# Performance work log

Measured on AMD Instinct MI355X. Metric: run time of the kernel, lower is better.

## Reference

```python
import jax, jax.numpy as jnp
import numpy as np

B, N, H, NH, P = 32, 400, 512, 8, 3
DK = H // NH
SCALE = DK ** -0.5
EPS = 1e-5


def _ln(x, g, b):
    m = jnp.mean(x, axis=-1, keepdims=True)
    v = jnp.mean((x - m) ** 2, axis=-1, keepdims=True)
    return (x - m) * jax.lax.rsqrt(v + EPS) * g + b


def _split(x):  # [B,N,H] -> [B,h,N,dk]
    return x.reshape(x.shape[0], x.shape[1], NH, DK).transpose(0, 2, 1, 3)


def _merge(x):  # [B,h,N,dk] -> [B,N,H]
    return x.transpose(0, 2, 1, 3).reshape(x.shape[0], x.shape[2], H)


def _attn(q, k, v, mask):
    s = jnp.einsum('bhid,bhjd->bhij', q, k) * SCALE
    s = s * (1.0 + mask[:, None])  # learned multiplicative prior mask
    p = jax.nn.softmax(s, axis=-1)
    return jnp.einsum('bhij,bhjd->bhid', p, v)


def _weight_gen(pri, z, C, wq, keys, wf, bf):
    # pooled token query attends over the num_priors prior matrices
    qv = jnp.mean(z @ wq, axis=1)  # [B,H]
    aw = jax.nn.softmax((qv @ keys.T) * (H ** -0.5), axis=-1)  # [B,P]
    w = jnp.einsum('bp,bpij->bij', aw, pri)  # [B,N,N] fused prior mask
    fused = jnp.einsum('bij,bjh->bih', C, z) @ wf + bf  # [B,N,H] neighborhood fusion
    return w, aw, fused


def _ffn(x, w1, b1, w2, b2):
    return jax.nn.gelu(x @ w1 + b1, approximate=False) @ w2 + b2


def _forward(x_FC, x_SC, pri_FC, pri_SC, FC, SC, dw,
             ln_attn_FC_g, ln_attn_FC_b, ln_attn_SC_g, ln_attn_SC_b,
             ln_ffn_FC_g, ln_ffn_FC_b, ln_ffn_SC_g, ln_ffn_SC_b,
             qkv_FC_w, qkv_SC_w,
             ffn_FC_w1, ffn_FC_b1, ffn_FC_w2, ffn_FC_b2,
             ffn_SC_w1, ffn_SC_b1, ffn_SC_w2, ffn_SC_b2,
             wg_q_w, wg_keys, wg_fuse_w, wg_fuse_b,
             dist_in_FC_w, dist_in_FC_b, dist_in_SC_w, dist_in_SC_b,
             dist_out_FC_w, dist_out_FC_b, dist_out_SC_w, dist_out_SC_b):
    z_FC = _ln(x_FC, ln_attn_FC_g, ln_attn_FC_b)
    z_SC = _ln(x_SC, ln_attn_SC_g, ln_attn_SC_b)
    q_FC, k_FC, v_FC = [_split(t) for t in jnp.split(z_FC @ qkv_FC_w, 3, axis=-1)]
    q_SC, k_SC, v_SC = [_split(t) for t in jnp.split(z_SC @ qkv_SC_w, 3, axis=-1)]
    w_FC, aw_FC, fused_FC = _weight_gen(pri_FC, z_FC, FC, wg_q_w, wg_keys, wg_fuse_w, wg_fuse_b)
    w_SC, aw_SC, fused_SC = _weight_gen(pri_SC, z_SC, SC, wg_q_w, wg_keys, wg_fuse_w, wg_fuse_b)
    ctx_FC = _merge(_attn(q_FC, k_FC, v_FC, w_FC))
    ctx_SC = _merge(_attn(q_SC, k_SC, v_SC, w_SC))
    attn_out_FC = x_FC + ctx_FC + fused_FC
    attn_out_SC = x_SC + ctx_SC + fused_SC
    x_FC_new = attn_out_FC + _ffn(_ln(attn_out_FC, ln_ffn_FC_g, ln_ffn_FC_b), ffn_FC_w1, ffn_FC_b1, ffn_FC_w2, ffn_FC_b2)
    x_SC_new = attn_out_SC + _ffn(_ln(attn_out_SC, ln_ffn_SC_g, ln_ffn_SC_b), ffn_SC_w1, ffn_SC_b1, ffn_SC_w2, ffn_SC_b2)
    wf, ws = dw[0], dw[1]
    proj_FC = x_FC_new @ dist_in_FC_w + dist_in_FC_b
    proj_SC = x_SC_new @ dist_in_SC_w + dist_in_SC_b
    l_FC = jax.nn.log_softmax(proj_FC.reshape(-1, H), axis=-1)
    l_SC = jax.nn.log_softmax(proj_SC.reshape(-1, H), axis=-1)
    p_FC = jnp.exp(l_FC)
    p_SC = jnp.exp(l_SC)
    rows = jnp.float32(l_FC.shape[0])
    kl_FC = jnp.sum(p_SC * (l_SC - l_FC)) / rows  # KLDiv(batchmean)(l_FC, p_SC)
    kl_SC = jnp.sum(p_FC * (l_FC - l_SC)) / rows
    x_FC_out = (1.0 - wf) * x_FC_new + wf * (proj_FC @ dist_out_FC_w + dist_out_FC_b)
    x_SC_out = (1.0 - ws) * x_SC_new + ws * (proj_SC @ dist_out_SC_w + dist_out_SC_b)
    distill_loss = 0.5 * (kl_FC * wf + kl_SC * ws)
    return (x_FC_out, x_SC_out, distill_loss, aw_FC, aw_SC)


def setup_inputs() -> dict:
    key = jax.random.key(0)
    ks = jax.random.split(key, 24)
    init = lambda k, shape: 0.02 * jax.random.normal(k, shape, jnp.float32)
    d = {}
    d['x_FC'] = jax.random.normal(ks[0], (B, N, H), jnp.float32)
    d['x_SC'] = jax.random.normal(ks[1], (B, N, H), jnp.float32)
    d['pri_FC'] = jax.random.uniform(ks[2], (B, P, N, N), jnp.float32)
    d['pri_SC'] = jax.random.uniform(ks[3], (B, P, N, N), jnp.float32)
    d['FC'] = jax.random.uniform(ks[4], (B, N, N), jnp.float32)
    d['SC'] = jax.random.uniform(ks[5], (B, N, N), jnp.float32)
    d['dw'] = jnp.array([0.5, 0.5], jnp.float32)
    for nm in ['ln_attn_FC', 'ln_attn_SC', 'ln_ffn_FC', 'ln_ffn_SC']:
        d[nm + '_g'] = jnp.ones((H,), jnp.float32)
        d[nm + '_b'] = jnp.zeros((H,), jnp.float32)
    d['qkv_FC_w'] = init(ks[6], (H, 3 * H))
    d['qkv_SC_w'] = init(ks[7], (H, 3 * H))
    d['ffn_FC_w1'] = init(ks[8], (H, 4 * H)); d['ffn_FC_b1'] = jnp.zeros((4 * H,), jnp.float32)
    d['ffn_FC_w2'] = init(ks[9], (4 * H, H)); d['ffn_FC_b2'] = jnp.zeros((H,), jnp.float32)
    d['ffn_SC_w1'] = init(ks[10], (H, 4 * H)); d['ffn_SC_b1'] = jnp.zeros((4 * H,), jnp.float32)
    d['ffn_SC_w2'] = init(ks[11], (4 * H, H)); d['ffn_SC_b2'] = jnp.zeros((H,), jnp.float32)
    d['wg_q_w'] = init(ks[12], (H, H))
    d['wg_keys'] = init(ks[13], (P, H))
    d['wg_fuse_w'] = init(ks[14], (H, H)); d['wg_fuse_b'] = jnp.zeros((H,), jnp.float32)
    d['dist_in_FC_w'] = init(ks[15], (H, H)); d['dist_in_FC_b'] = jnp.zeros((H,), jnp.float32)
    d['dist_in_SC_w'] = init(ks[16], (H, H)); d['dist_in_SC_b'] = jnp.zeros((H,), jnp.float32)
    d['dist_out_FC_w'] = init(ks[17], (H, H)); d['dist_out_FC_b'] = jnp.zeros((H,), jnp.float32)
    d['dist_out_SC_w'] = init(ks[18], (H, H)); d['dist_out_SC_b'] = jnp.zeros((H,), jnp.float32)
    return d


def reference(x_FC, x_SC, pri_FC, pri_SC, FC, SC, dw,
              ln_attn_FC_g, ln_attn_FC_b, ln_attn_SC_g, ln_attn_SC_b,
              ln_ffn_FC_g, ln_ffn_FC_b, ln_ffn_SC_g, ln_ffn_SC_b,
              qkv_FC_w, qkv_SC_w,
              ffn_FC_w1, ffn_FC_b1, ffn_FC_w2, ffn_FC_b2,
              ffn_SC_w1, ffn_SC_b1, ffn_SC_w2, ffn_SC_b2,
              wg_q_w, wg_keys, wg_fuse_w, wg_fuse_b,
              dist_in_FC_w, dist_in_FC_b, dist_in_SC_w, dist_in_SC_b,
              dist_out_FC_w, dist_out_FC_b, dist_out_SC_w, dist_out_SC_b):
    return _forward(x_FC, x_SC, pri_FC, pri_SC, FC, SC, dw,
                    ln_attn_FC_g, ln_attn_FC_b, ln_attn_SC_g, ln_attn_SC_b,
                    ln_ffn_FC_g, ln_ffn_FC_b, ln_ffn_SC_g, ln_ffn_SC_b,
                    qkv_FC_w, qkv_SC_w,
                    ffn_FC_w1, ffn_FC_b1, ffn_FC_w2, ffn_FC_b2,
                    ffn_SC_w1, ffn_SC_b1, ffn_SC_w2, ffn_SC_b2,
                    wg_q_w, wg_keys, wg_fuse_w, wg_fuse_b,
                    dist_in_FC_w, dist_in_FC_b, dist_in_SC_w, dist_in_SC_b,
                    dist_out_FC_w, dist_out_FC_b, dist_out_SC_w, dist_out_SC_b)
```

## Files before the change

### kernel.cpp

```cpp
#include <hip/hip_runtime.h>
#include <hip/hip_bf16.h>
#include <math.h>

typedef __hip_bfloat16 bf16;

#define B_  32
#define N_  400
#define H_  512
#define NH_ 8
#define DK_ 64
#define P_  3
#define BN_ (B_*N_)
#define H3_ 1536
#define H4_ 2048

#define GLD16(g, l) __builtin_amdgcn_global_load_lds( \
    (__attribute__((address_space(1))) void*)(g), \
    (__attribute__((address_space(3))) void*)(l), 16, 0, 0)

__device__ __forceinline__ float b2f(bf16 v){ return __bfloat162float(v); }
__device__ __forceinline__ bf16  f2b(float v){ return __float2bfloat16(v); }
__device__ __forceinline__ float bfu(unsigned short u){ return __uint_as_float(((unsigned int)u)<<16); }
__device__ __forceinline__ unsigned short f2bu(float v){
  union { bf16 b; unsigned short u; } cv; cv.b = __float2bfloat16(v); return cv.u;
}
__device__ __forceinline__ bool is_f32(const void* gref){
  return *(const unsigned int*)gref == 0x3F800000u;
}
__device__ __forceinline__ float ldRaw(const void* p, long i, bool f32){
  return f32 ? ((const float*)p)[i] : b2f(((const bf16*)p)[i]);
}
__device__ __forceinline__ void stRaw(void* p, long i, float v, bool f32){
  if (f32) ((float*)p)[i] = v; else ((bf16*)p)[i] = f2b(v);
}
__device__ __forceinline__ float gelu_t(float v){
  float y = 0.7978845608028654f*(v + 0.044715f*v*v*v);
  float ay = fabsf(y);
  float e = __expf(-2.f*ay);
  float th = (1.f - e)/(1.f + e);
  th = copysignf(th, y);
  return 0.5f*v*(1.f + th);
}

__device__ __forceinline__ float waveSum(float v){
  #pragma unroll
  for (int o=32;o>0;o>>=1) v += __shfl_xor(v,o,64);
  return v;
}
__device__ __forceinline__ float waveMax(float v){
  #pragma unroll
  for (int o=32;o>0;o>>=1) v = fmaxf(v,__shfl_xor(v,o,64));
  return v;
}
__device__ __forceinline__ float blockSum(float v, float* wred){
  v = waveSum(v);
  int w = threadIdx.x>>6, l = threadIdx.x&63;
  if (l==0) wred[w]=v;
  __syncthreads();
  float r = wred[0]+wred[1]+wred[2]+wred[3];
  __syncthreads();
  return r;
}
__device__ __forceinline__ float blockMax(float v, float* wred){
  v = waveMax(v);
  int w = threadIdx.x>>6, l = threadIdx.x&63;
  if (l==0) wred[w]=v;
  __syncthreads();
  float r = fmaxf(fmaxf(wred[0],wred[1]),fmaxf(wred[2],wred[3]));
  __syncthreads();
  return r;
}

template<int XMODE>
__global__ __launch_bounds__(256)
void ln_kernel(const void* __restrict__ x, const void* __restrict__ g,
               const void* __restrict__ bb, bf16* __restrict__ out,
               const void* __restrict__ gref)
{
  __shared__ float wred[4];
  const bool F32 = is_f32(gref);
  long row = blockIdx.x;
  int t = threadIdx.x;
  long base = row*H_;
  float v0, v1;
  if (XMODE==0){ v0 = ldRaw(x, base+t, F32); v1 = ldRaw(x, base+t+256, F32); }
  else         { v0 = b2f(((const bf16*)x)[base+t]); v1 = b2f(((const bf16*)x)[base+t+256]); }
  float mean = blockSum(v0+v1, wred) * (1.f/512.f);
  float d0 = v0-mean, d1 = v1-mean;
  float var = blockSum(d0*d0+d1*d1, wred) * (1.f/512.f);
  float rs = rsqrtf(var + 1e-5f);
  bf16* orow = out + base;
  orow[t]     = f2b(d0*rs*ldRaw(g,t,F32)     + ldRaw(bb,t,F32));
  orow[t+256] = f2b(d1*rs*ldRaw(g,t+256,F32) + ldRaw(bb,t+256,F32));
}

struct TC6 {
  const float* W[6];
  bf16* WT[6];
  int K[6]; int N[6]; int base[6];
};
__global__ __launch_bounds__(256)
void tc6_kernel(TC6 p)
{
  __shared__ float tile[32][33];
  int gt = blockIdx.x;
  int seg = 0;
  #pragma unroll
  for (int i=1;i<6;++i) if (gt >= p.base[i]) seg = i;
  int lt = gt - p.base[seg];
  int K = p.K[seg], N = p.N[seg];
  int ntx = N >> 5;
  int n0 = (lt % ntx)*32, k0 = (lt / ntx)*32;
  const float* W = p.W[seg];
  bf16* WT = p.WT[seg];
  int t = threadIdx.x;
  int c = t & 31, r = t >> 5;
  #pragma unroll
  for (int q=0;q<4;++q){
    int k = r + q*8;
    tile[k][c] = W[(long)(k0+k)*N + n0 + c];
  }
  __syncthreads();
  #pragma unroll
  for (int q=0;q<4;++q){
    int nn = r + q*8;
    WT[(long)(n0+nn)*K + k0 + c] = f2b(tile[c][nn]);
  }
}

__global__ __launch_bounds__(256)
void ztrans_kernel(const bf16* __restrict__ ZB, bf16* __restrict__ ZBT)
{
  __shared__ unsigned short tile[32][33];
  int j0 = blockIdx.x*32, h0 = blockIdx.y*32, b = blockIdx.z;
  int t = threadIdx.x;
  int c = t & 31, r = t >> 5;
  const unsigned short* src = (const unsigned short*)(ZB + (long)b*N_*H_);
  #pragma unroll
  for (int p=0;p<4;++p){
    int j = j0 + r + p*8;
    unsigned short v = 0;
    if (j < 400) v = src[(long)j*H_ + h0 + c];
    tile[r+p*8][c] = v;
  }
  __syncthreads();
  unsigned short* dst = (unsigned short*)(ZBT + (long)b*512*416);
  #pragma unroll
  for (int p=0;p<4;++p){
    int hh = r + p*8;
    dst[(long)(h0+hh)*416 + j0 + c] = tile[c][hh];
  }
}

__global__ __launch_bounds__(256)
void cconv_kernel(const float* __restrict__ C, bf16* __restrict__ CB)
{
  long u = ((long)blockIdx.x*256 + threadIdx.x)*8;
  int b = (int)(u / (512*416));
  int rem = (int)(u - (long)b*(512*416));
  int r = rem / 416, c = rem % 416;
  ushort4 lo = {0,0,0,0}, hi = {0,0,0,0};
  if (r < 400 && c < 400){
    const float* p = C + (long)b*160000 + r*400 + c;
    float4 f0 = *(const float4*)p;
    float4 f1 = *(const float4*)(p+4);
    lo.x=f2bu(f0.x); lo.y=f2bu(f0.y); lo.z=f2bu(f0.z); lo.w=f2bu(f0.w);
    hi.x=f2bu(f1.x); hi.y=f2bu(f1.y); hi.z=f2bu(f1.z); hi.w=f2bu(f1.w);
  }
  *(ushort4*)((unsigned short*)CB + u)     = lo;
  *(ushort4*)((unsigned short*)CB + u + 4) = hi;
}

__global__ __launch_bounds__(256)
void vtrans_kernel(const bf16* __restrict__ qkv, bf16* __restrict__ vtg)
{
  __shared__ unsigned short tile[32][33];
  int j0 = blockIdx.x*32, d0 = blockIdx.y*32, bh = blockIdx.z;
  int b = bh >> 3, h = bh & 7;
  int t = threadIdx.x;
  int c = t & 31, r = t >> 5;
  const unsigned short* src = (const unsigned short*)(qkv + (long)b*N_*H3_ + 1024 + h*64 + d0);
  #pragma unroll
  for (int p=0;p<4;++p){
    int j = j0 + r + p*8;
    unsigned short v = 0;
    if (j < 400) v = src[(long)j*H3_ + c];
    tile[r+p*8][c] = v;
  }
  __syncthreads();
  unsigned short* dst = (unsigned short*)(vtg + (long)bh*64*416);
  #pragma unroll
  for (int p=0;p<4;++p){
    int dd = r + p*8;
    dst[(long)(d0+dd)*416 + j0 + c] = tile[c][dd];
  }
}

template<int MI,int ACT,int RES,int OMODE>
__global__ __launch_bounds__(256)
void mgemm_kernel(const bf16* __restrict__ A, const bf16* __restrict__ BT,
                  const float* __restrict__ bias, const bf16* __restrict__ res,
                  void* __restrict__ out, long oOff,
                  int M, int K, int Nn,
                  long sA, long sW, long sO,
                  const float* __restrict__ dwp, int dwidx)
{
  typedef __attribute__((ext_vector_type(8))) short bf16x8;
  typedef __attribute__((ext_vector_type(4))) float f32x4;
  constexpr int BM = MI*32;
  constexpr int LPT = MI/2 + 2;
  __shared__ unsigned short As[3][BM*32];
  __shared__ unsigned short Bs[3][128*32];
  unsigned nbx = gridDim.x, nby = gridDim.y;
  long nb = (long)nbx*nby*gridDim.z;
  long hw = blockIdx.x + (long)nbx*(blockIdx.y + (long)nby*blockIdx.z);
  long tid2 = (hw & 7)*(nb >> 3) + (hw >> 3);
  int bx = (int)(tid2 % nbx);
  long r2 = tid2 / nbx;
  int by = (int)(r2 % nby);
  int bz = (int)(r2 / nby);

  int t = threadIdx.x;
  int w = t >> 6, l = t & 63;
  int wm = (w >> 1)*(MI*16), wn = (w & 1)*64;
  int m0 = by*BM, n0 = bx*128;
  const bf16* Ab = A + (long)bz*sA;
  const bf16* Bb = BT + (long)bz*sW;
  long zO = (long)bz*sO;
  f32x4 acc[MI][4] = {};
  int lrow = l & 15, lkc = l >> 4;
  int srow = t >> 2, skc = t & 3;
  int sk = (skc ^ ((srow >> 1) & 3))*8;
  int ck = (lkc ^ ((lrow >> 1) & 3))*8;
  int nk = K >> 5;

  auto STAGE = [&](int tile, int bufi){
    int kk = tile << 5;
    #pragma unroll
    for (int half=0; half<MI/2; ++half){
      const unsigned short* gA = (const unsigned short*)Ab + (long)(m0+srow+half*64)*K + kk + sk;
      GLD16(gA, &As[bufi][w*512 + half*2048]);
    }
    #pragma unroll
    for (int half=0; half<2; ++half){
      const unsigned short* gB = (const unsigned short*)Bb + (long)(n0+srow+half*64)*K + kk + sk;
      GLD16(gB, &Bs[bufi][w*512 + half*2048]);
    }
  };

  STAGE(0, 0);
  if (nk > 1) STAGE(1, 1);
  for (int kt=0; kt<nk; ++kt){
    int cur = kt % 3;
    if (kt+2 < nk) STAGE(kt+2, (kt+2)%3);
    if (kt+2 < nk)      asm volatile("s_waitcnt vmcnt(%0)" :: "i"(2*LPT) : "memory");
    else if (kt+1 < nk) asm volatile("s_waitcnt vmcnt(%0)" :: "i"(LPT)   : "memory");
    else                asm volatile("s_waitcnt vmcnt(0)" ::: "memory");
    __builtin_amdgcn_s_barrier();
    asm volatile("" ::: "memory");
    bf16x8 af[MI], bf_[4];
    #pragma unroll
    for (int i=0;i<MI;++i) af[i]  = *(const bf16x8*)&As[cur][(wm + i*16 + lrow)*32 + ck];
    #pragma unroll
    for (int i=0;i<4;++i)  bf_[i] = *(const bf16x8*)&Bs[cur][(wn + i*16 + lrow)*32 + ck];
    __builtin_amdgcn_s_setprio(1);
    #pragma unroll
    for (int mi=0;mi<MI;++mi)
      #pragma unroll
      for (int ni=0;ni<4;++ni)
        acc[mi][ni] = __builtin_amdgcn_mfma_f32_16x16x32_bf16(bf_[ni], af[mi], acc[mi][ni], 0, 0, 0);
    __builtin_amdgcn_s_setprio(0);
    asm volatile("" ::: "memory");
    __builtin_amdgcn_s_barrier();
  }
  float wbl = (RES==2) ? dwp[dwidx] : 0.f;
  #pragma unroll
  for (int mi=0;mi<MI;++mi){
    int gm = m0 + wm + mi*16 + lrow;
    if (gm >= M) continue;
    #pragma unroll
    for (int ni=0;ni<4;++ni){
      int gnb = n0 + wn + ni*16 + lkc*4;
      long o = zO + (long)gm*Nn + gnb;
      float v0 = acc[mi][ni][0], v1 = acc[mi][ni][1], v2 = acc[mi][ni][2], v3 = acc[mi][ni][3];
      if (bias){
        float4 bv = *(const float4*)&bias[gnb];
        v0 += bv.x; v1 += bv.y; v2 += bv.z; v3 += bv.w;
      }
      if (ACT==1){
        v0 = gelu_t(v0); v1 = gelu_t(v1); v2 = gelu_t(v2); v3 = gelu_t(v3);
      }
      if (RES==1){
        ushort4 r4 = *(const ushort4*)((const unsigned short*)res + o);
        v0 += bfu(r4.x); v1 += bfu(r4.y); v2 += bfu(r4.z); v3 += bfu(r4.w);
      }
      if (RES==2){
        ushort4 r4 = *(const ushort4*)((const unsigned short*)res + o);
        v0 = (1.f-wbl)*bfu(r4.x) + wbl*v0;
        v1 = (1.f-wbl)*bfu(r4.y) + wbl*v1;
        v2 = (1.f-wbl)*bfu(r4.z) + wbl*v2;
        v3 = (1.f-wbl)*bfu(r4.w) + wbl*v3;
      }
      if (OMODE==0){
        ushort4 o4;
        o4.x = f2bu(v0); o4.y = f2bu(v1); o4.z = f2bu(v2); o4.w = f2bu(v3);
        *(ushort4*)((unsigned short*)out + o) = o4;
      } else {
        *(float4*)((float*)out + oOff + o) = make_float4(v0,v1,v2,v3);
      }
    }
  }
}

__global__ __launch_bounds__(256)
void zbar_kernel(const bf16* __restrict__ Z, float* __restrict__ zbar)
{
  __shared__ float red[256];
  int hc = blockIdx.x, b = blockIdx.y;
  int t = threadIdx.x;
  int col = hc*64 + (t & 63), ns = t >> 6;
  const bf16* p = Z + (long)b*N_*H_ + (long)ns*100*H_ + col;
  float s = 0.f;
  for (int n=0;n<100;++n) s += b2f(p[(long)n*H_]);
  red[t] = s;
  __syncthreads();
  if (t < 64){
    float tot = red[t]+red[t+64]+red[t+128]+red[t+192];
    zbar[b*512 + hc*64 + t] = tot * (1.f/400.f);
  }
}

__global__ __launch_bounds__(256)
void qv_kernel(const float* __restrict__ zbar, const void* __restrict__ wq,
               float* __restrict__ qv, const void* __restrict__ gref)
{
  __shared__ float red[256];
  const bool F32 = is_f32(gref);
  int ch = blockIdx.x, b = blockIdx.y;
  int t = threadIdx.x;
  int col = ch*32 + (t & 31), ks = t >> 5;
  const float* zb = zbar + b*512;
  float s = 0.f;
  int k0 = ks*64;
  for (int k=0;k<64;++k)
    s = fmaf(zb[k0+k], ldRaw(wq, (long)(k0+k)*512 + col, F32), s);
  red[t] = s;
  __syncthreads();
  if (t < 32){
    float q = 0.f;
    #pragma unroll
    for (int i=0;i<8;++i) q += red[t + i*32];
    qv[b*512 + ch*32 + t] = q;
  }
}

__global__ __launch_bounds__(256)
void aw_kernel(const float* __restrict__ qv, const void* __restrict__ keys,
               float* __restrict__ awf, void* __restrict__ outbase, long offAw,
               const void* __restrict__ gref)
{
  __shared__ float wred[4];
  const bool F32 = is_f32(gref);
  int b = blockIdx.x, t = threadIdx.x;
  const float* q = qv + b*512;
  float lg[3];
  #pragma unroll
  for (int p=0;p<3;++p){
    float part = q[t]*ldRaw(keys, p*512+t, F32) + q[t+256]*ldRaw(keys, p*512+t+256, F32);
    lg[p] = blockSum(part, wred) * 0.04419417382415922f;
  }
  float m = fmaxf(lg[0], fmaxf(lg[1], lg[2]));
  float e0 = expf(lg[0]-m), e1 = expf(lg[1]-m), e2 = expf(lg[2]-m);
  float inv = 1.f/(e0+e1+e2);
  if (t<3){
    float a = (t==0?e0:(t==1?e1:e2))*inv;
    awf[b*3+t] = a;
    stRaw(outbase, offAw + b*3 + t, a, F32);
  }
}

__global__ __launch_bounds__(256)
void wcomb_kernel(const void* __restrict__ pri, const float* __restrict__ awf,
                  bf16* __restrict__ WM, const void* __restrict__ gref)
{
  const bool F32 = is_f32(gref);
  long u = (long)blockIdx.x*256 + threadIdx.x;
  long e0 = u*4;
  int b = (int)(e0 / 160000);
  long r = e0 - (long)b*160000;
  float a0 = awf[b*3+0], a1 = awf[b*3+1], a2 = awf[b*3+2];
  float o0,o1,o2,o3;
  if (F32){
    const float* p0 = (const float*)pri + (long)b*3*160000 + r;
    float4 a = *(const float4*)(p0);
    float4 c = *(const float4*)(p0 + 160000);
    float4 d = *(const float4*)(p0 + 320000);
    o0 = a0*a.x + a1*c.x + a2*d.x;
    o1 = a0*a.y + a1*c.y + a2*d.y;
    o2 = a0*a.z + a1*c.z + a2*d.z;
    o3 = a0*a.w + a1*c.w + a2*d.w;
  } else {
    const bf16* p0 = (const bf16*)pri + (long)b*3*160000 + r;
    ushort4 a = *(const ushort4*)(p0);
    ushort4 c = *(const ushort4*)(p0 + 160000);
    ushort4 d = *(const ushort4*)(p0 + 320000);
    o0 = a0*bfu(a.x) + a1*bfu(c.x) + a2*bfu(d.x);
    o1 = a0*bfu(a.y) + a1*bfu(c.y) + a2*bfu(d.y);
    o2 = a0*bfu(a.z) + a1*bfu(c.z) + a2*bfu(d.z);
    o3 = a0*bfu(a.w) + a1*bfu(c.w) + a2*bfu(d.w);
  }
  ushort4 o;
  o.x = f2bu(o0); o.y = f2bu(o1); o.z = f2bu(o2); o.w = f2bu(o3);
  *(ushort4*)(WM + e0) = o;
}

__global__ __launch_bounds__(128)
void attn_kernel(const bf16* __restrict__ qkv, const bf16* __restrict__ wm,
                 const bf16* __restrict__ vtg, const void* __restrict__ x,
                 const bf16* __restrict__ fused, bf16* __restrict__ aout,
                 const void* __restrict__ gref)
{
  typedef __attribute__((ext_vector_type(8))) short bf16x8;
  typedef __attribute__((ext_vector_type(4))) float f32x4;
  __shared__ unsigned short Pbuf[2][2][16*40];
  const bool F32 = is_f32(gref);
  int t = threadIdx.x, wv = t >> 6, l = t & 63;
  int h = blockIdx.x, b = blockIdx.y;
  int qt = blockIdx.z*2 + wv;
  if (qt >= 25) return;
  int lr = l & 15, lg = l >> 4;
  int i0 = qt*16;
  const bf16* qb = qkv + (long)b*N_*H3_ + h*64;
  const bf16* kb = qb + 512;
  const bf16* wrow = wm + (long)b*N_*N_ + (long)(i0+lr)*400 + lg*4;
  const bf16* vt = vtg + (long)(b*NH_ + h)*64*416;
  bf16x8 qf0 = *(const bf16x8*)(qb + (long)(i0+lr)*H3_ + lg*8);
  bf16x8 qf1 = *(const bf16x8*)(qb + (long)(i0+lr)*H3_ + 32 + lg*8);
  bf16x8 ka0, ka1, kc0, kc1, vp0, vp1, vp2, vp3;
  uint2 ma, mc;
  ka0 = *(const bf16x8*)(kb + (long)(0*16+lr)*H3_ + lg*8);
  ka1 = *(const bf16x8*)(kb + (long)(0*16+lr)*H3_ + 32 + lg*8);
  kc0 = *(const bf16x8*)(kb + (long)(1*16+lr)*H3_ + lg*8);
  kc1 = *(const bf16x8*)(kb + (long)(1*16+lr)*H3_ + 32 + lg*8);
  ma = *(const uint2*)(wrow + 0*16);
  mc = *(const uint2*)(wrow + 1*16);
  vp0 = *(const bf16x8*)(vt + (long)( 0+lr)*416 + lg*8);
  vp1 = *(const bf16x8*)(vt + (long)(16+lr)*416 + lg*8);
  vp2 = *(const bf16x8*)(vt + (long)(32+lr)*416 + lg*8);
  vp3 = *(const bf16x8*)(vt + (long)(48+lr)*416 + lg*8);
  float rm = -1e30f, rl = 0.f;
  f32x4 o[4] = {};
  #pragma unroll
  for (int w=0; w<13; ++w){
    f32x4 s0 = {0.f,0.f,0.f,0.f}, s1;
    s0 = __builtin_amdgcn_mfma_f32_16x16x32_bf16(ka0, qf0, s0, 0,0,0);
    s0 = __builtin_amdgcn_mfma_f32_16x16x32_bf16(ka1, qf1, s0, 0,0,0);
    if (w < 12){
      f32x4 z = {0.f,0.f,0.f,0.f};
      z = __builtin_amdgcn_mfma_f32_16x16x32_bf16(kc0, qf0, z, 0,0,0);
      z = __builtin_amdgcn_mfma_f32_16x16x32_bf16(kc1, qf1, z, 0,0,0);
      s1 = z;
    }
    s0[0] = s0[0]*0.125f*(1.f + bfu((unsigned short)(ma.x & 0xffffu)));
    s0[1] = s0[1]*0.125f*(1.f + bfu((unsigned short)(ma.x >> 16)));
    s0[2] = s0[2]*0.125f*(1.f + bfu((unsigned short)(ma.y & 0xffffu)));
    s0[3] = s0[3]*0.125f*(1.f + bfu((unsigned short)(ma.y >> 16)));
    if (w < 12){
      s1[0] = s1[0]*0.125f*(1.f + bfu((unsigned short)(mc.x & 0xffffu)));
      s1[1] = s1[1]*0.125f*(1.f + bfu((unsigned short)(mc.x >> 16)));
      s1[2] = s1[2]*0.125f*(1.f + bfu((unsigned short)(mc.y & 0xffffu)));
      s1[3] = s1[3]*0.125f*(1.f + bfu((unsigned short)(mc.y >> 16)));
    } else {
      s1[0]=s1[1]=s1[2]=s1[3] = -1e30f;
    }
    bf16x8 na0, na1, nc0, nc1, nv0, nv1, nv2, nv3;
    uint2 nma, nmc;
    if (w < 12){
      int t0n = 2*w+2, t1n = 2*w+3;
      na0 = *(const bf16x8*)(kb + (long)(t0n*16+lr)*H3_ + lg*8);
      na1 = *(const bf16x8*)(kb + (long)(t0n*16+lr)*H3_ + 32 + lg*8);
      nma = *(const uint2*)(wrow + t0n*16);
      if (w < 11){
        nc0 = *(const bf16x8*)(kb + (long)(t1n*16+lr)*H3_ + lg*8);
        nc1 = *(const bf16x8*)(kb + (long)(t1n*16+lr)*H3_ + 32 + lg*8);
        nmc = *(const uint2*)(wrow + t1n*16);
      }
      int wn1 = (w+1)*32;
      nv0 = *(const bf16x8*)(vt + (long)( 0+lr)*416 + wn1 + lg*8);
      nv1 = *(const bf16x8*)(vt + (long)(16+lr)*416 + wn1 + lg*8);
      nv2 = *(const bf16x8*)(vt + (long)(32+lr)*416 + wn1 + lg*8);
      nv3 = *(const bf16x8*)(vt + (long)(48+lr)*416 + wn1 + lg*8);
    }
    float tm = fmaxf(fmaxf(fmaxf(s0[0],s0[1]), fmaxf(s0[2],s0[3])),
                     fmaxf(fmaxf(s1[0],s1[1]), fmaxf(s1[2],s1[3])));
    tm = fmaxf(tm, __shfl_xor(tm, 16));
    tm = fmaxf(tm, __shfl_xor(tm, 32));
    float mn = fmaxf(rm, tm);
    float sc = __expf(rm - mn);
    unsigned pk0x, pk0y, pk1x = 0u, pk1y = 0u;
    float ls = 0.f;
    {
      unsigned u0 = f2bu(__expf(s0[0]-mn)), u1 = f2bu(__expf(s0[1]-mn));
      unsigned u2 = f2bu(__expf(s0[2]-mn)), u3 = f2bu(__expf(s0[3]-mn));
      pk0x = u0 | (u1<<16); pk0y = u2 | (u3<<16);
      ls += __uint_as_float(u0<<16) + __uint_as_float(u1<<16)
          + __uint_as_float(u2<<16) + __uint_as_float(u3<<16);
    }
    if (w < 12){
      unsigned u0 = f2bu(__expf(s1[0]-mn)), u1 = f2bu(__expf(s1[1]-mn));
      unsigned u2 = f2bu(__expf(s1[2]-mn)), u3 = f2bu(__expf(s1[3]-mn));
      pk1x = u0 | (u1<<16); pk1y = u2 | (u3<<16);
      ls += __uint_as_float(u0<<16) + __uint_as_float(u1<<16)
          + __uint_as_float(u2<<16) + __uint_as_float(u3<<16);
    }
    ls += __shfl_xor(ls, 16);
    ls += __shfl_xor(ls, 32);
    rl = rl*sc + ls;
    rm = mn;
    unsigned short* pb = Pbuf[wv][w & 1];
    *(uint2*)&pb[lr*40 + lg*4]      = make_uint2(pk0x, pk0y);
    *(uint2*)&pb[lr*40 + 16 + lg*4] = make_uint2(pk1x, pk1y);
    bf16x8 pa = *(const bf16x8*)&pb[lr*40 + lg*8];
    float sq0 = __shfl(sc, lg*4 + 0);
    float sq1 = __shfl(sc, lg*4 + 1);
    float sq2 = __shfl(sc, lg*4 + 2);
    float sq3 = __shfl(sc, lg*4 + 3);
    o[0][0] *= sq0; o[0][1] *= sq1; o[0][2] *= sq2; o[0][3] *= sq3;
    o[0] = __builtin_amdgcn_mfma_f32_16x16x32_bf16(pa, vp0, o[0], 0,0,0);
    o[1][0] *= sq0; o[1][1] *= sq1; o[1][2] *= sq2; o[1][3] *= sq3;
    o[1] = __builtin_amdgcn_mfma_f32_16x16x32_bf16(pa, vp1, o[1], 0,0,0);
    o[2][0] *= sq0; o[2][1] *= sq1; o[2][2] *= sq2; o[2][3] *= sq3;
    o[2] = __builtin_amdgcn_mfma_f32_16x16x32_bf16(pa, vp2, o[2], 0,0,0);
    o[3][0] *= sq0; o[3][1] *= sq1; o[3][2] *= sq2; o[3][3] *= sq3;
    o[3] = __builtin_amdgcn_mfma_f32_16x16x32_bf16(pa, vp3, o[3], 0,0,0);
    if (w < 12){
      ka0 = na0; ka1 = na1; ma = nma;
      if (w < 11){ kc0 = nc0; kc1 = nc1; mc = nmc; }
      vp0 = nv0; vp1 = nv1; vp2 = nv2; vp3 = nv3;
    }
  }
  float invl = 1.f/rl;
  #pragma unroll
  for (int q=0;q<4;++q){
    float iv = __shfl(invl, lg*4 + q);
    long gi = (long)(b*N_ + i0 + lg*4 + q);
    #pragma unroll
    for (int dt=0;dt<4;++dt){
      long oi = gi*H_ + h*64 + dt*16 + lr;
      float xv = F32 ? ((const float*)x)[oi] : b2f(((const bf16*)x)[oi]);
      float fv = b2f(fused[oi]);
      aout[oi] = f2b(o[dt][q]*iv + xv + fv);
    }
  }
}

__global__ __launch_bounds__(256)
void kl_rows_kernel(const bf16* __restrict__ pF, const bf16* __restrict__ pS,
                    float2* __restrict__ rowpart)
{
  __shared__ float wred[4];
  long row = blockIdx.x;
  int t = threadIdx.x;
  const bf16* fr = pF + row*512;
  const bf16* sr = pS + row*512;
  float f0 = b2f(fr[t]), f1 = b2f(fr[t+256]), s0 = b2f(sr[t]), s1 = b2f(sr[t+256]);
  float mF = blockMax(fmaxf(f0,f1), wred);
  float mS = blockMax(fmaxf(s0,s1), wred);
  float sumF = blockSum(__expf(f0-mF)+__expf(f1-mF), wred);
  float sumS = blockSum(__expf(s0-mS)+__expf(s1-mS), wred);
  float lseF = mF + __logf(sumF), lseS = mS + __logf(sumS);
  float lF0 = f0-lseF, lF1 = f1-lseF, lS0 = s0-lseS, lS1 = s1-lseS;
  float pS0 = __expf(lS0), pS1 = __expf(lS1), pF0 = __expf(lF0), pF1 = __expf(lF1);
  float a  = pS0*(lS0-lF0) + pS1*(lS1-lF1);
  float bb = pF0*(lF0-lS0) + pF1*(lF1-lS1);
  a  = blockSum(a,  wred);
  bb = blockSum(bb, wred);
  if (t==0) rowpart[row] = make_float2(a, bb);
}

__global__ __launch_bounds__(256)
void kl_final_kernel(const float2* __restrict__ rowpart, const void* __restrict__ dw,
                     void* __restrict__ outbase, long offLoss,
                     const void* __restrict__ gref)
{
  __shared__ float wred[4];
  const bool F32 = is_f32(gref);
  int t = threadIdx.x;
  float sa=0.f, sb=0.f;
  for (int i=t;i<BN_;i+=256){ float2 v = rowpart[i]; sa+=v.x; sb+=v.y; }
  sa = blockSum(sa, wred);
  sb = blockSum(sb, wred);
  if (t==0){
    float wf = ldRaw(dw,0,F32), ws = ldRaw(dw,1,F32);
    float loss = 0.5f*((sa/12800.f)*wf + (sb/12800.f)*ws);
    stRaw(outbase, offLoss, loss, F32);
  }
}

#define OFF_ZB    0L
#define OFF_QKV   13107200L
#define OFF_FUSED 52428800L
#define OFF_WM    65536000L
#define OFF_CZ    75776000L
#define OFF_PROJ0 88883200L
#define OFF_PROJ1 101990400L
#define OFF_QKVT  115097600L
#define OFF_W1T   116670464L
#define OFF_W2T   118767616L
#define OFF_FUT   120864768L
#define OFF_DIT   121389056L
#define OFF_DOT   121913344L
#define OFF_ZBT   122437632L
#define OFF_ZBAR  136069120L
#define OFF_AWF   136134656L
#define OFF_ROWP  136135680L
#define OFF_VTG   136238080L
#define OFF_QV    149869568L

extern "C" void kernel_launch(void* const* d_in, const int* in_sizes, int n_in,
                              void* d_out, int out_size, void* d_ws, size_t ws_size,
                              hipStream_t stream)
{
  (void)in_sizes; (void)n_in; (void)out_size; (void)ws_size;
  const void* x[2]    = {d_in[0],  d_in[1]};
  const void* pri[2]  = {d_in[2],  d_in[3]};
  const float* Cm[2]  = {(const float*)d_in[4], (const float*)d_in[5]};
  const float* dwf    =  (const float*)d_in[6];
  const void* lnag[2] = {d_in[7],  d_in[9]};
  const void* lnab[2] = {d_in[8],  d_in[10]};
  const void* lnfg[2] = {d_in[11], d_in[13]};
  const void* lnfb[2] = {d_in[12], d_in[14]};
  const float* qkvw[2]= {(const float*)d_in[15], (const float*)d_in[16]};
  const float* fw1[2] = {(const float*)d_in[17], (const float*)d_in[21]};
  const float* fb1[2] = {(const float*)d_in[18], (const float*)d_in[22]};
  const float* fw2[2] = {(const float*)d_in[19], (const float*)d_in[23]};
  const float* fb2[2] = {(const float*)d_in[20], (const float*)d_in[24]};
  const void* wgq     =  d_in[25];
  const void* wgk     =  d_in[26];
  const float* wgfw   =  (const float*)d_in[27];
  const float* wgfb   =  (const float*)d_in[28];
  const float* diw[2] = {(const float*)d_in[29], (const float*)d_in[31]};
  const float* dib[2] = {(const float*)d_in[30], (const float*)d_in[32]};
  const float* dow[2] = {(const float*)d_in[33], (const float*)d_in[35]};
  const float* dob[2] = {(const float*)d_in[34], (const float*)d_in[36]};
  const void* gref    =  d_in[7];

  char* ws = (char*)d_ws;
  bf16*  ZB    = (bf16*)(ws + OFF_ZB);
  bf16*  LN2   = (bf16*)(ws + OFF_ZB);
  bf16*  XNEW  = (bf16*)(ws + OFF_ZB);
  bf16*  QKV   = (bf16*)(ws + OFF_QKV);
  bf16*  HH    = (bf16*)(ws + OFF_QKV);
  bf16*  FUSED = (bf16*)(ws + OFF_FUSED);
  bf16*  WM    = (bf16*)(ws + OFF_WM);
  bf16*  CZ    = (bf16*)(ws + OFF_CZ);
  bf16*  AOUT  = (bf16*)(ws + OFF_CZ);
  bf16*  PROJ[2] = {(bf16*)(ws + OFF_PROJ0), (bf16*)(ws + OFF_PROJ1)};
  bf16*  QKVT  = (bf16*)(ws + OFF_QKVT);
  bf16*  W1T   = (bf16*)(ws + OFF_W1T);
  bf16*  W2T   = (bf16*)(ws + OFF_W2T);
  bf16*  FUT   = (bf16*)(ws + OFF_FUT);
  bf16*  DIT   = (bf16*)(ws + OFF_DIT);
  bf16*  DOT   = (bf16*)(ws + OFF_DOT);
  bf16*  ZBT   = (bf16*)(ws + OFF_ZBT);
  bf16*  VTG   = (bf16*)(ws + OFF_VTG);
  bf16*  CB    = (bf16*)(ws + OFF_VTG);
  float* ZBAR  = (float*)(ws + OFF_ZBAR);
  float* AWF   = (float*)(ws + OFF_AWF);
  float2* ROWP = (float2*)(ws + OFF_ROWP);
  float* QV    = (float*)(ws + OFF_QV);

  const long offX[2]  = {0L, 6553600L};
  const long offLoss  = 13107200L;
  const long offAw[2] = {13107201L, 13107297L};

  for (int s=0; s<2; ++s){
    TC6 tp;
    tp.W[0]=qkvw[s]; tp.WT[0]=QKVT; tp.K[0]=512;  tp.N[0]=1536;
    tp.W[1]=fw1[s];  tp.WT[1]=W1T;  tp.K[1]=512;  tp.N[1]=2048;
    tp.W[2]=fw2[s];  tp.WT[2]=W2T;  tp.K[2]=2048; tp.N[2]=512;
    tp.W[3]=wgfw;    tp.WT[3]=FUT;  tp.K[3]=512;  tp.N[3]=512;
    tp.W[4]=diw[s];  tp.WT[4]=DIT;  tp.K[4]=512;  tp.N[4]=512;
    tp.W[5]=dow[s];  tp.WT[5]=DOT;  tp.K[5]=512;  tp.N[5]=512;
    tp.base[0]=0; tp.base[1]=768; tp.base[2]=1792; tp.base[3]=2816;
    tp.base[4]=3072; tp.base[5]=3328;
    tc6_kernel<<<3584,256,0,stream>>>(tp);
    ln_kernel<0><<<BN_,256,0,stream>>>(x[s], lnag[s], lnab[s], ZB, gref);
    zbar_kernel<<<dim3(8,B_),256,0,stream>>>(ZB, ZBAR);
    ztrans_kernel<<<dim3(13,16,32),256,0,stream>>>(ZB, ZBT);
    cconv_kernel<<<3328,256,0,stream>>>(Cm[s], CB);
    mgemm_kernel<4,0,0,0><<<dim3(12,100,1),256,0,stream>>>(
        ZB, QKVT, nullptr, nullptr, QKV, 0, BN_, 512, H3_, 0,0,0, nullptr,0);
    qv_kernel<<<dim3(16,B_),256,0,stream>>>(ZBAR, wgq, QV, gref);
    aw_kernel<<<B_,256,0,stream>>>(QV, wgk, AWF, d_out, offAw[s], gref);
    wcomb_kernel<<<5000,256,0,stream>>>(pri[s], AWF, WM, gref);
    mgemm_kernel<4,0,0,0><<<dim3(4,4,32),256,0,stream>>>(
        CB, ZBT, nullptr, nullptr, CZ, 0, 400, 416, 512,
        212992L, 212992L, 204800L, nullptr,0);
    mgemm_kernel<2,0,0,0><<<dim3(4,200,1),256,0,stream>>>(
        CZ, FUT, wgfb, nullptr, FUSED, 0, BN_, 512, 512, 0,0,0, nullptr,0);
    vtrans_kernel<<<dim3(13,2,256),256,0,stream>>>(QKV, VTG);
    attn_kernel<<<dim3(NH_,B_,13),128,0,stream>>>(QKV, WM, VTG, x[s], FUSED, AOUT, gref);
    ln_kernel<1><<<BN_,256,0,stream>>>(AOUT, lnfg[s], lnfb[s], LN2, gref);
    mgemm_kernel<4,1,0,0><<<dim3(16,100,1),256,0,stream>>>(
        LN2, W1T, fb1[s], nullptr, HH, 0, BN_, 512, H4_, 0,0,0, nullptr,0);
    mgemm_kernel<2,0,1,0><<<dim3(4,200,1),256,0,stream>>>(
        HH, W2T, fb2[s], AOUT, XNEW, 0, BN_, 2048, 512, 0,0,0, nullptr,0);
    mgemm_kernel<2,0,0,0><<<dim3(4,200,1),256,0,stream>>>(
        XNEW, DIT, dib[s], nullptr, PROJ[s], 0, BN_, 512, 512, 0,0,0, nullptr,0);
    mgemm_kernel<2,0,2,1><<<dim3(4,200,1),256,0,stream>>>(
        PROJ[s], DOT, dob[s], XNEW, d_out, offX[s], BN_, 512, 512, 0,0,0, dwf, s);
  }
  kl_rows_kernel<<<BN_,256,0,stream>>>(PROJ[0], PROJ[1], ROWP);
  kl_final_kernel<<<1,256,0,stream>>>(ROWP, dwf, d_out, offLoss, gref);
}
```

Baseline: 850.8 us.

## Fold wq·keysᵀ into a precomputed matrix and fuse C conversion into weight prep

The prior-weight logits are computed by first forming WK = wq @ keysᵀ (512x3) in a small kernel. A single per-batch kernel then reduces z against WK directly, replacing the zbar, qv and aw kernels. This removes two launches and the 512x512 matvec per batch. The C fp32→bf16 conversion is merged into the weight transpose kernel as extra blocks, and attn_kernel gets a min-blocks-per-CU launch bound. The trade-off is a different summation order, plus the awdirect kernel running only 32 blocks that each stream a full batch of z serially.

```diff
diff --git a/kernel.cpp b/kernel.cpp
--- a/kernel.cpp
+++ b/kernel.cpp
@@ -100,10 +100,27 @@
   int K[6]; int N[6]; int base[6];
 };
 __global__ __launch_bounds__(256)
-void tc6_kernel(TC6 p)
+void prep_kernel(TC6 p, const float* __restrict__ C, bf16* __restrict__ CB)
 {
   __shared__ float tile[32][33];
   int gt = blockIdx.x;
+  if (gt >= 3584){
+    long u = ((long)(gt-3584)*256 + threadIdx.x)*8;
+    int b = (int)(u / (512*416));
+    int rem = (int)(u - (long)b*(512*416));
+    int r = rem / 416, c = rem % 416;
+    ushort4 lo = {0,0,0,0}, hi = {0,0,0,0};
+    if (r < 400 && c < 400){
+      const float* pp = C + (long)b*160000 + r*400 + c;
+      float4 f0 = *(const float4*)pp;
+      float4 f1 = *(const float4*)(pp+4);
+      lo.x=f2bu(f0.x); lo.y=f2bu(f0.y); lo.z=f2bu(f0.z); lo.w=f2bu(f0.w);
+      hi.x=f2bu(f1.x); hi.y=f2bu(f1.y); hi.z=f2bu(f1.z); hi.w=f2bu(f1.w);
+    }
+    *(ushort4*)((unsigned short*)CB + u)     = lo;
+    *(ushort4*)((unsigned short*)CB + u + 4) = hi;
+    return;
+  }
   int seg = 0;
   #pragma unroll
   for (int i=1;i<6;++i) if (gt >= p.base[i]) seg = i;
@@ -150,25 +167,6 @@
     int hh = r + p*8;
     dst[(long)(h0+hh)*416 + j0 + c] = tile[c][hh];
   }
-}
-
-__global__ __launch_bounds__(256)
-void cconv_kernel(const float* __restrict__ C, bf16* __restrict__ CB)
-{
-  long u = ((long)blockIdx.x*256 + threadIdx.x)*8;
-  int b = (int)(u / (512*416));
-  int rem = (int)(u - (long)b*(512*416));
-  int r = rem / 416, c = rem % 416;
-  ushort4 lo = {0,0,0,0}, hi = {0,0,0,0};
-  if (r < 400 && c < 400){
-    const float* p = C + (long)b*160000 + r*400 + c;
-    float4 f0 = *(const float4*)p;
-    float4 f1 = *(const float4*)(p+4);
-    lo.x=f2bu(f0.x); lo.y=f2bu(f0.y); lo.z=f2bu(f0.z); lo.w=f2bu(f0.w);
-    hi.x=f2bu(f1.x); hi.y=f2bu(f1.y); hi.z=f2bu(f1.z); hi.w=f2bu(f1.w);
-  }
-  *(ushort4*)((unsigned short*)CB + u)     = lo;
-  *(ushort4*)((unsigned short*)CB + u + 4) = hi;
 }
 
 __global__ __launch_bounds__(256)
@@ -312,65 +310,57 @@
   }
 }
 
-__global__ __launch_bounds__(256)
-void zbar_kernel(const bf16* __restrict__ Z, float* __restrict__ zbar)
-{
-  __shared__ float red[256];
-  int hc = blockIdx.x, b = blockIdx.y;
-  int t = threadIdx.x;
-  int col = hc*64 + (t & 63), ns = t >> 6;
-  const bf16* p = Z + (long)b*N_*H_ + (long)ns*100*H_ + col;
-  float s = 0.f;
-  for (int n=0;n<100;++n) s += b2f(p[(long)n*H_]);
-  red[t] = s;
-  __syncthreads();
-  if (t < 64){
-    float tot = red[t]+red[t+64]+red[t+128]+red[t+192];
-    zbar[b*512 + hc*64 + t] = tot * (1.f/400.f);
-  }
-}
-
-__global__ __launch_bounds__(256)
-void qv_kernel(const float* __restrict__ zbar, const void* __restrict__ wq,
-               float* __restrict__ qv, const void* __restrict__ gref)
-{
-  __shared__ float red[256];
+__global__ __launch_bounds__(64)
+void wk_kernel(const void* __restrict__ wq, const void* __restrict__ keys,
+               float* __restrict__ WK, const void* __restrict__ gref)
+{
   const bool F32 = is_f32(gref);
-  int ch = blockIdx.x, b = blockIdx.y;
-  int t = threadIdx.x;
-  int col = ch*32 + (t & 31), ks = t >> 5;
-  const float* zb = zbar + b*512;
-  float s = 0.f;
-  int k0 = ks*64;
-  for (int k=0;k<64;++k)
-    s = fmaf(zb[k0+k], ldRaw(wq, (long)(k0+k)*512 + col, F32), s);
-  red[t] = s;
-  __syncthreads();
-  if (t < 32){
-    float q = 0.f;
-    #pragma unroll
-    for (int i=0;i<8;++i) q += red[t + i*32];
-    qv[b*512 + ch*32 + t] = q;
-  }
-}
-
-__global__ __launch_bounds__(256)
-void aw_kernel(const float* __restrict__ qv, const void* __restrict__ keys,
-               float* __restrict__ awf, void* __restrict__ outbase, long offAw,
-               const void* __restrict__ gref)
-{
+  int k = blockIdx.x;
+  int l = threadIdx.x;
+  float s0=0.f, s1=0.f, s2=0.f;
+  for (int j=l; j<512; j+=64){
+    float w = ldRaw(wq, (long)k*512 + j, F32);
+    s0 = fmaf(w, ldRaw(keys, 0*512+j, F32), s0);
+    s1 = fmaf(w, ldRaw(keys, 1*512+j, F32), s1);
+    s2 = fmaf(w, ldRaw(keys, 2*512+j, F32), s2);
+  }
+  s0 = waveSum(s0); s1 = waveSum(s1); s2 = waveSum(s2);
+  if (l==0){ WK[k*3+0]=s0; WK[k*3+1]=s1; WK[k*3+2]=s2; }
+}
+
+__global__ __launch_bounds__(256)
+void awdirect_kernel(const bf16* __restrict__ Z, const float* __restrict__ WK,
+                     float* __restrict__ awf, void* __restrict__ outbase, long offAw,
+                     const void* __restrict__ gref)
+{
+  __shared__ float wk[1536];
   __shared__ float wred[4];
   const bool F32 = is_f32(gref);
   int b = blockIdx.x, t = threadIdx.x;
-  const float* q = qv + b*512;
-  float lg[3];
-  #pragma unroll
-  for (int p=0;p<3;++p){
-    float part = q[t]*ldRaw(keys, p*512+t, F32) + q[t+256]*ldRaw(keys, p*512+t+256, F32);
-    lg[p] = blockSum(part, wred) * 0.04419417382415922f;
-  }
-  float m = fmaxf(lg[0], fmaxf(lg[1], lg[2]));
-  float e0 = expf(lg[0]-m), e1 = expf(lg[1]-m), e2 = expf(lg[2]-m);
+  for (int i=t; i<1536; i+=256) wk[i] = WK[i];
+  __syncthreads();
+  const unsigned short* zb = (const unsigned short*)(Z + (long)b*N_*H_);
+  float a0=0.f, a1=0.f, a2=0.f;
+  for (int base = t*8; base < 204800; base += 2048){
+    ushort4 lo = *(const ushort4*)(zb + base);
+    ushort4 hi = *(const ushort4*)(zb + base + 4);
+    int k = base & 511;
+    float zv[8] = {bfu(lo.x),bfu(lo.y),bfu(lo.z),bfu(lo.w),
+                   bfu(hi.x),bfu(hi.y),bfu(hi.z),bfu(hi.w)};
+    #pragma unroll
+    for (int j=0;j<8;++j){
+      a0 = fmaf(zv[j], wk[(k+j)*3+0], a0);
+      a1 = fmaf(zv[j], wk[(k+j)*3+1], a1);
+      a2 = fmaf(zv[j], wk[(k+j)*3+2], a2);
+    }
+  }
+  a0 = blockSum(a0, wred);
+  a1 = blockSum(a1, wred);
+  a2 = blockSum(a2, wred);
+  float sc = 0.04419417382415922f / 400.f;
+  float lg0=a0*sc, lg1=a1*sc, lg2=a2*sc;
+  float m = fmaxf(lg0, fmaxf(lg1, lg2));
+  float e0=__expf(lg0-m), e1=__expf(lg1-m), e2=__expf(lg2-m);
   float inv = 1.f/(e0+e1+e2);
   if (t<3){
     float a = (t==0?e0:(t==1?e1:e2))*inv;
@@ -414,7 +404,7 @@
   *(ushort4*)(WM + e0) = o;
 }
 
-__global__ __launch_bounds__(128)
+__global__ __launch_bounds__(128, 4)
 void attn_kernel(const bf16* __restrict__ qkv, const bf16* __restrict__ wm,
                  const bf16* __restrict__ vtg, const void* __restrict__ x,
                  const bf16* __restrict__ fused, bf16* __restrict__ aout,
@@ -611,7 +601,7 @@
 #define OFF_DIT   121389056L
 #define OFF_DOT   121913344L
 #define OFF_ZBT   122437632L
-#define OFF_ZBAR  136069120L
+#define OFF_WK    136069120L
 #define OFF_AWF   136134656L
 #define OFF_ROWP  136135680L
 #define OFF_VTG   136238080L
@@ -665,10 +655,9 @@
   bf16*  ZBT   = (bf16*)(ws + OFF_ZBT);
   bf16*  VTG   = (bf16*)(ws + OFF_VTG);
   bf16*  CB    = (bf16*)(ws + OFF_VTG);
-  float* ZBAR  = (float*)(ws + OFF_ZBAR);
+  float* WK    = (float*)(ws + OFF_WK);
   float* AWF   = (float*)(ws + OFF_AWF);
   float2* ROWP = (float2*)(ws + OFF_ROWP);
-  float* QV    = (float*)(ws + OFF_QV);
 
   const long offX[2]  = {0L, 6553600L};
   const long offLoss  = 13107200L;
@@ -684,15 +673,13 @@
     tp.W[5]=dow[s];  tp.WT[5]=DOT;  tp.K[5]=512;  tp.N[5]=512;
     tp.base[0]=0; tp.base[1]=768; tp.base[2]=1792; tp.base[3]=2816;
     tp.base[4]=3072; tp.base[5]=3328;
-    tc6_kernel<<<3584,256,0,stream>>>(tp);
+    prep_kernel<<<6912,256,0,stream>>>(tp, Cm[s], CB);
+    wk_kernel<<<512,64,0,stream>>>(wgq, wgk, WK, gref);
     ln_kernel<0><<<BN_,256,0,stream>>>(x[s], lnag[s], lnab[s], ZB, gref);
-    zbar_kernel<<<dim3(8,B_),256,0,stream>>>(ZB, ZBAR);
     ztrans_kernel<<<dim3(13,16,32),256,0,stream>>>(ZB, ZBT);
-    cconv_kernel<<<3328,256,0,stream>>>(Cm[s], CB);
     mgemm_kernel<4,0,0,0><<<dim3(12,100,1),256,0,stream>>>(
         ZB, QKVT, nullptr, nullptr, QKV, 0, BN_, 512, H3_, 0,0,0, nullptr,0);
-    qv_kernel<<<dim3(16,B_),256,0,stream>>>(ZBAR, wgq, QV, gref);
-    aw_kernel<<<B_,256,0,stream>>>(QV, wgk, AWF, d_out, offAw[s], gref);
+    awdirect_kernel<<<B_,256,0,stream>>>(ZB, WK, AWF, d_out, offAw[s], gref);
     wcomb_kernel<<<5000,256,0,stream>>>(pri[s], AWF, WM, gref);
     mgemm_kernel<4,0,0,0><<<dim3(4,4,32),256,0,stream>>>(
         CB, ZBT, nullptr, nullptr, CZ, 0, 400, 416, 512,
```

New measurement: 879.9 us. 1.03x slower.
